# Kernel optimization log

Measured on AMD Instinct MI355X. Metric: run time of the kernel, lower is better.

## Reference

```python
import jax, jax.numpy as jnp
import numpy as np

HEADS = 1
WC = 32  # weight_channels (weights shared across channel groups via c % WC)
K1 = 3
K2 = 5
PAD1 = 1
PAD2 = 2


def _patches(x, k, pad):
    # x: [N, C, H, W] -> [N, C, k*k, H, W], zero padding, stride 1, dilation 1
    N, C, H, W = x.shape
    xp = jnp.pad(x, ((0, 0), (0, 0), (pad, pad), (pad, pad)))
    ps = [xp[:, :, i:i + H, j:j + W] for i in range(k) for j in range(k)]
    return jnp.stack(ps, axis=2)


def setup_inputs() -> dict:
    key = jax.random.key(0)
    k1, k2 = jax.random.split(key)
    x = jax.random.normal(k1, (2, 256, 64, 64), dtype=jnp.float32)
    # weight layout: [N, heads*WC*(K1*K1 + K2*K2), H, W] = [2, 1*32*(9+25), 64, 64]
    weight = jax.random.normal(k2, (2, HEADS * WC * (K1 * K1 + K2 * K2), 64, 64), dtype=jnp.float32)
    return {"x": x, "weight": weight}


def reference(x, weight):
    N, C, H, W = x.shape
    g = C // WC  # channel groups sharing the same per-pixel weights
    n1 = HEADS * WC * K1 * K1
    w1 = weight[:, :n1].reshape(N, HEADS, WC, K1 * K1, H, W)
    w2 = weight[:, n1:].reshape(N, HEADS, WC, K2 * K2, H, W)

    p1 = _patches(x, K1, PAD1).reshape(N, g, WC, K1 * K1, H, W)
    p2 = _patches(x, K2, PAD2).reshape(N, g, WC, K2 * K2, H, W)

    out1 = jnp.einsum('ngckhw,nackhw->nagchw', p1, w1).reshape(N, HEADS, C, H, W)
    out2 = jnp.einsum('ngckhw,nackhw->nagchw', p2, w2).reshape(N, HEADS, C, H, W)
    # top layout: [N, kernel_num=2, heads, C, H, W]
    return jnp.stack([out1, out2], axis=1)
```

## Files before the change

### kernel.cpp

```cpp
#include <hip/hip_runtime.h>


#define HW_ (64 * 64)

__global__ __launch_bounds__(256) void lconv_mix_kernel(
    const float* __restrict__ x, const float* __restrict__ wgt,
    float* __restrict__ out) {
  int idx = blockIdx.x * blockDim.x + threadIdx.x;
  int w  = idx & 63;
  int h  = (idx >> 6) & 63;
  int wc = (idx >> 12) & 31;
  int n  = idx >> 17;

  const float* wbase = wgt + (size_t)n * 1088 * HW_ + h * 64 + w;

  float w1[9];
  float w2[25];
#pragma unroll
  for (int t = 0; t < 9; ++t) w1[t] = wbase[(size_t)(wc * 9 + t) * HW_];
#pragma unroll
  for (int t = 0; t < 25; ++t) w2[t] = wbase[(size_t)(288 + wc * 25 + t) * HW_];

  const float* xn = x + (size_t)n * 256 * HW_;
  float* o1 = out + ((size_t)(n * 2 + 0) * 256) * HW_ + h * 64 + w;
  float* o2 = out + ((size_t)(n * 2 + 1) * 256) * HW_ + h * 64 + w;

#pragma unroll
  for (int g = 0; g < 8; ++g) {
    int cc = g * 32 + wc;
    const float* xc = xn + (size_t)cc * HW_;

    float v[5][5];
#pragma unroll
    for (int i = 0; i < 5; ++i) {
      int hh = h + i - 2;
      bool hok = (hh >= 0) & (hh < 64);
#pragma unroll
      for (int j = 0; j < 5; ++j) {
        int ww = w + j - 2;
        bool ok = hok & (ww >= 0) & (ww < 64);
        v[i][j] = ok ? xc[hh * 64 + ww] : 0.0f;
      }
    }

    float a1 = 0.0f;
#pragma unroll
    for (int i = 0; i < 3; ++i)
#pragma unroll
      for (int j = 0; j < 3; ++j)
        a1 = fmaf(v[i + 1][j + 1], w1[i * 3 + j], a1);

    float a2 = 0.0f;
#pragma unroll
    for (int i = 0; i < 5; ++i)
#pragma unroll
      for (int j = 0; j < 5; ++j)
        a2 = fmaf(v[i][j], w2[i * 5 + j], a2);

    o1[(size_t)cc * HW_] = a1;
    o2[(size_t)cc * HW_] = a2;
  }
}

extern "C" void kernel_launch(void* const* d_in, const int* in_sizes, int n_in,
                              void* d_out, int out_size, void* d_ws,
                              size_t ws_size, hipStream_t stream) {
  const float* x = (const float*)d_in[0];
  const float* wgt = (const float*)d_in[1];
  float* out = (float*)d_out;

  int total = 2 * 32 * 64 * 64;
  dim3 block(256);
  dim3 grid(total / 256);
  lconv_mix_kernel<<<grid, block, 0, stream>>>(x, wgt, out);
}
```

Before: 92.25 us.

## Share horizontal stencil neighbors via wavefront DPP shifts instead of redundant loads

Each thread now loads only the 5 vertically offset x values for its column. It gets the horizontal neighbours at offsets -2..+2 through wavefront-wide DPP shift-left and shift-right operations. Because a wave64 covers exactly one 64-wide row, the zero fill on out-of-range lanes supplies the left and right padding. This cuts global load instructions per channel from 25 to 5, and weight loads and output stores now use nontemporal hints to reduce cache pollution. The correctness of the shuffle depends on the wave being 64 lanes and mapping one image row.

```diff
diff --git a/kernel.cpp b/kernel.cpp
--- a/kernel.cpp
+++ b/kernel.cpp
@@ -1,7 +1,18 @@
 #include <hip/hip_runtime.h>
 
 
-#define HW_ (64 * 64)
+#define HW_ 4096
+
+__device__ __forceinline__ float dpp_shl1(float v) {
+  return __builtin_bit_cast(
+      float, __builtin_amdgcn_update_dpp(0, __builtin_bit_cast(int, v),
+                                         0x130, 0xF, 0xF, true));
+}
+__device__ __forceinline__ float dpp_shr1(float v) {
+  return __builtin_bit_cast(
+      float, __builtin_amdgcn_update_dpp(0, __builtin_bit_cast(int, v),
+                                         0x138, 0xF, 0xF, true));
+}
 
 __global__ __launch_bounds__(256) void lconv_mix_kernel(
     const float* __restrict__ x, const float* __restrict__ wgt,
@@ -13,15 +24,15 @@
   int n  = idx >> 17;
 
   const float* wbase = wgt + (size_t)n * 1088 * HW_ + h * 64 + w;
+  float w1[9], w2[25];
+#pragma unroll
+  for (int t = 0; t < 9; ++t)
+    w1[t] = __builtin_nontemporal_load(&wbase[(size_t)(wc * 9 + t) * HW_]);
+#pragma unroll
+  for (int t = 0; t < 25; ++t)
+    w2[t] = __builtin_nontemporal_load(&wbase[(size_t)(288 + wc * 25 + t) * HW_]);
 
-  float w1[9];
-  float w2[25];
-#pragma unroll
-  for (int t = 0; t < 9; ++t) w1[t] = wbase[(size_t)(wc * 9 + t) * HW_];
-#pragma unroll
-  for (int t = 0; t < 25; ++t) w2[t] = wbase[(size_t)(288 + wc * 25 + t) * HW_];
-
-  const float* xn = x + (size_t)n * 256 * HW_;
+  const float* xn = x + (size_t)n * 256 * HW_ + h * 64 + w;
   float* o1 = out + ((size_t)(n * 2 + 0) * 256) * HW_ + h * 64 + w;
   float* o2 = out + ((size_t)(n * 2 + 1) * 256) * HW_ + h * 64 + w;
 
@@ -30,35 +41,36 @@
     int cc = g * 32 + wc;
     const float* xc = xn + (size_t)cc * HW_;
 
-    float v[5][5];
+    float r[5];
 #pragma unroll
     for (int i = 0; i < 5; ++i) {
       int hh = h + i - 2;
-      bool hok = (hh >= 0) & (hh < 64);
+      r[i] = ((unsigned)hh < 64u) ? xc[(i - 2) * 64] : 0.0f;
+    }
+
+    float a1 = 0.0f, a2 = 0.0f;
 #pragma unroll
-      for (int j = 0; j < 5; ++j) {
-        int ww = w + j - 2;
-        bool ok = hok & (ww >= 0) & (ww < 64);
-        v[i][j] = ok ? xc[hh * 64 + ww] : 0.0f;
+    for (int i = 0; i < 5; ++i) {
+      float m1 = dpp_shr1(r[i]);
+      float m2 = dpp_shr1(m1);
+      float q1 = dpp_shl1(r[i]);
+      float q2 = dpp_shl1(q1);
+
+      a2 = fmaf(m2,   w2[i * 5 + 0], a2);
+      a2 = fmaf(m1,   w2[i * 5 + 1], a2);
+      a2 = fmaf(r[i], w2[i * 5 + 2], a2);
+      a2 = fmaf(q1,   w2[i * 5 + 3], a2);
+      a2 = fmaf(q2,   w2[i * 5 + 4], a2);
+
+      if (i >= 1 && i <= 3) {
+        a1 = fmaf(m1,   w1[(i - 1) * 3 + 0], a1);
+        a1 = fmaf(r[i], w1[(i - 1) * 3 + 1], a1);
+        a1 = fmaf(q1,   w1[(i - 1) * 3 + 2], a1);
       }
     }
 
-    float a1 = 0.0f;
-#pragma unroll
-    for (int i = 0; i < 3; ++i)
-#pragma unroll
-      for (int j = 0; j < 3; ++j)
-        a1 = fmaf(v[i + 1][j + 1], w1[i * 3 + j], a1);
-
-    float a2 = 0.0f;
-#pragma unroll
-    for (int i = 0; i < 5; ++i)
-#pragma unroll
-      for (int j = 0; j < 5; ++j)
-        a2 = fmaf(v[i][j], w2[i * 5 + j], a2);
-
-    o1[(size_t)cc * HW_] = a1;
-    o2[(size_t)cc * HW_] = a2;
+    __builtin_nontemporal_store(a1, &o1[(size_t)cc * HW_]);
+    __builtin_nontemporal_store(a2, &o2[(size_t)cc * HW_]);
   }
 }
 
@@ -70,7 +82,5 @@
   float* out = (float*)d_out;
 
   int total = 2 * 32 * 64 * 64;
-  dim3 block(256);
-  dim3 grid(total / 256);
-  lconv_mix_kernel<<<grid, block, 0, stream>>>(x, wgt, out);
+  lconv_mix_kernel<<<dim3(total / 256), dim3(256), 0, stream>>>(x, wgt, out);
 }
```

Result: no change. 93.05 us (+0.9%).
